# Optimization experiments

Measured on AMD Instinct MI355X. Metric: run time of the kernel, lower is better.

The kernel has to match this reference:

```python
import jax, jax.numpy as jnp
import numpy as np

WINDOW = 11
SIGMA = 1.5
K1 = 0.01
K2 = 0.03
L = 1.0


def _gauss_kernel(dtype):
    coords = jnp.arange(WINDOW, dtype=dtype) - (WINDOW - 1) / 2.0
    g = jnp.exp(-coords ** 2 / (2.0 * SIGMA ** 2))
    g = g / g.sum()
    return jnp.outer(g, g)  # [k, k]


def setup_inputs() -> dict:
    key = jax.random.key(0)
    k1, k2 = jax.random.split(key)
    B, T, H, W = 8, 16, 256, 256
    return {
        "predicted": jax.random.normal(k1, (B, T, H, W, 1), dtype=jnp.float32),
        "target": jax.random.normal(k2, (B, T, H, W, 1), dtype=jnp.float32),
    }


def reference(predicted, target):
    B, T, H, W, C = predicted.shape
    dt = predicted.dtype
    eps = jnp.asarray(1e-6, dt)

    # valid mask: samples whose target sums to zero are excluded (weighted mean)
    valid = (jnp.sum(target, axis=(1, 2, 3, 4)) != 0).astype(dt)  # [B]

    # per-sample, per-channel min-max normalization over (T, H, W)
    def norm(x):
        mn = jnp.min(x, axis=(1, 2, 3), keepdims=True)
        mx = jnp.max(x, axis=(1, 2, 3), keepdims=True)
        return (x - mn) / jnp.maximum(mx - mn, eps)

    p = norm(predicted)
    t = norm(target)

    # batch all (B,T) single-channel images through one conv: NCHW with N = B*T
    img1 = t.reshape(B * T, 1, H, W)  # original uses target as img1
    img2 = p.reshape(B * T, 1, H, W)
    kern = _gauss_kernel(dt).reshape(1, 1, WINDOW, WINDOW)
    pad = WINDOW // 2

    def conv(x):
        return jax.lax.conv_general_dilated(x, kern, (1, 1), [(pad, pad), (pad, pad)])

    mu1 = conv(img1)
    mu2 = conv(img2)
    mu1_sq = mu1 * mu1
    mu2_sq = mu2 * mu2
    mu1_mu2 = mu1 * mu2
    sigma1_sq = jnp.maximum(conv(img1 * img1) - mu1_sq, eps)
    sigma2_sq = jnp.maximum(conv(img2 * img2) - mu2_sq, eps)
    sigma12 = conv(img1 * img2) - mu1_mu2

    C1 = (K1 * L) ** 2
    C2 = (K2 * L) ** 2
    C3 = C2 / 2.0
    root = jnp.sqrt(sigma1_sq * sigma2_sq)
    luminance = (2.0 * mu1_mu2 + C1) / (mu1_sq + mu2_sq + C1)
    contrast = (2.0 * root + C2) / (sigma1_sq + sigma2_sq + C2)
    structure = (sigma12 + C3) / (root + C3)
    ssim_map = luminance * contrast * structure  # [B*T, 1, H, W]

    # per-(b,t) pixel mean, then mean over T == mean over (T,H,W)
    ssim_per_sample = ssim_map.reshape(B, T, H, W).mean(axis=(1, 2, 3))  # [B]

    n_valid = jnp.maximum(jnp.sum(valid), jnp.asarray(1.0, dt))
    loss = jnp.sum((1.0 - ssim_per_sample) * valid) / n_valid
    return loss
```

## Files before the change

### kernel.cpp

```cpp
#include <hip/hip_runtime.h>
#include <math.h>

#define BB 8
#define TT 16
#define HH 256
#define WW 256
#define NPX (TT * HH * WW)
#define CROWS 32
#define NBLK (BB * TT * (HH / CROWS))

#define P_MINP 0
#define P_MAXP 512
#define P_MINT 1024
#define P_MAXT 1536
#define P_SUMT 2048
#define WS_S   2560

typedef float v2f __attribute__((ext_vector_type(2)));

#define G0 0.0010283776f
#define G1 0.0075987582f
#define G2 0.0360008014f
#define G3 0.1093606427f
#define G4 0.2130055745f
#define G5 0.2660117857f
#define GA_(k) ((k) == 0 || (k) == 10 ? G0 : (k) == 1 || (k) == 9 ? G1 \
              : (k) == 2 || (k) == 8 ? G2 : (k) == 3 || (k) == 7 ? G3 \
              : (k) == 4 || (k) == 6 ? G4 : G5)

__global__ __launch_bounds__(256) void k_reduce(const float* __restrict__ p,
                                                const float* __restrict__ t,
                                                float* __restrict__ wsf) {
  const int b = blockIdx.x >> 6;
  const size_t base = (size_t)b * NPX + (size_t)(blockIdx.x & 63) * (NPX / 64);
  const int tid = threadIdx.x;

  float mnp = 3.4e38f, mxp = -3.4e38f, mnt = 3.4e38f, mxt = -3.4e38f, st = 0.f;
  const float4* p4 = (const float4*)(p + base);
  const float4* t4 = (const float4*)(t + base);
#pragma unroll 4
  for (int it = 0; it < 16; ++it) {
    float4 a = p4[it * 256 + tid];
    float4 c = t4[it * 256 + tid];
    mnp = fminf(mnp, fminf(fminf(a.x, a.y), fminf(a.z, a.w)));
    mxp = fmaxf(mxp, fmaxf(fmaxf(a.x, a.y), fmaxf(a.z, a.w)));
    mnt = fminf(mnt, fminf(fminf(c.x, c.y), fminf(c.z, c.w)));
    mxt = fmaxf(mxt, fmaxf(fmaxf(c.x, c.y), fmaxf(c.z, c.w)));
    st += c.x + c.y + c.z + c.w;
  }
  for (int off = 32; off > 0; off >>= 1) {
    mnp = fminf(mnp, __shfl_down(mnp, off));
    mxp = fmaxf(mxp, __shfl_down(mxp, off));
    mnt = fminf(mnt, __shfl_down(mnt, off));
    mxt = fmaxf(mxt, __shfl_down(mxt, off));
    st += __shfl_down(st, off);
  }
  __shared__ float s_mnp[4], s_mxp[4], s_mnt[4], s_mxt[4], s_st[4];
  int wave = tid >> 6, lane = tid & 63;
  if (lane == 0) {
    s_mnp[wave] = mnp; s_mxp[wave] = mxp;
    s_mnt[wave] = mnt; s_mxt[wave] = mxt; s_st[wave] = st;
  }
  __syncthreads();
  if (tid == 0) {
    for (int w = 1; w < 4; ++w) {
      mnp = fminf(mnp, s_mnp[w]); mxp = fmaxf(mxp, s_mxp[w]);
      mnt = fminf(mnt, s_mnt[w]); mxt = fmaxf(mxt, s_mxt[w]);
      st += s_st[w];
    }
    wsf[P_MINP + blockIdx.x] = mnp;
    wsf[P_MAXP + blockIdx.x] = mxp;
    wsf[P_MINT + blockIdx.x] = mnt;
    wsf[P_MAXT + blockIdx.x] = mxt;
    wsf[P_SUMT + blockIdx.x] = st;
    if (blockIdx.x == 0) wsf[WS_S] = 0.f;
  }
}

#define STEP(J) do {                                                         \
    constexpr int jj = (J);                                                  \
    constexpr int buf = jj & 1;                                              \
    constexpr int slot = jj % 11;                                            \
    const bool in = (unsigned)(ystart + jj) < (unsigned)HH;                  \
    v2f nv;                                                                  \
    nv.x = in ? fmaf(tcur, ts, tb) : 0.f;                                    \
    nv.y = in ? fmaf(pcur, ps, pb) : 0.f;                                    \
    srow[buf][x + 5] = nv;                                                   \
    if constexpr (jj < 41) {                                                 \
      const int yn = min(max(ystart + jj + 1, 0), HH - 1);                   \
      tnxt = tptr[(size_t)yn * WW + x];                                      \
      pnxt = pptr[(size_t)yn * WW + x];                                      \
    }                                                                        \
    __syncthreads();                                                         \
    v2f hmu = {0.f, 0.f}, hsq = {0.f, 0.f};                                  \
    float htp = 0.f;                                                         \
    _Pragma("unroll")                                                        \
    for (int k = 0; k < 11; ++k) {                                           \
      v2f v = srow[buf][x + k];                                              \
      v2f g2 = {GA_(k), GA_(k)};                                             \
      v2f w = g2 * v;                                                        \
      hmu = hmu + w;                                                         \
      hsq = __builtin_elementwise_fma(w, v, hsq);                            \
      htp = fmaf(w.x, v.y, htp);                                             \
    }                                                                        \
    r_mu[slot] = hmu; r_sq[slot] = hsq; r_tp[slot] = htp;                    \
    if constexpr (jj >= 10) {                                                \
      v2f vmu = {0.f, 0.f}, vsq = {0.f, 0.f};                                \
      float vtp = 0.f;                                                       \
      _Pragma("unroll")                                                      \
      for (int k = 0; k < 11; ++k) {                                         \
        const int s = (jj + 1 + k) % 11;                                     \
        v2f g2 = {GA_(k), GA_(k)};                                           \
        vmu = __builtin_elementwise_fma(g2, r_mu[s], vmu);                   \
        vsq = __builtin_elementwise_fma(g2, r_sq[s], vsq);                   \
        vtp = fmaf(GA_(k), r_tp[s], vtp);                                    \
      }                                                                      \
      float m1 = vmu.x, m2 = vmu.y;                                          \
      float mu11 = m1 * m1, mu22 = m2 * m2, m12 = m1 * m2;                   \
      float s1 = fmaxf(vsq.x - mu11, 1e-6f);                                 \
      float s2 = fmaxf(vsq.y - mu22, 1e-6f);                                 \
      float s12 = vtp - m12;                                                 \
      float root = sqrtf(s1 * s2);                                           \
      float num = fmaf(2.f, m12, C1) * fmaf(2.f, root, C2) * (s12 + C3);     \
      float den = (mu11 + mu22 + C1) * (s1 + s2 + C2) * (root + C3);         \
      acc = fmaf(num, __builtin_amdgcn_rcpf(den), acc);                      \
    }                                                                        \
    tcur = tnxt; pcur = pnxt;                                                \
    __builtin_amdgcn_sched_barrier(0);                                       \
  } while (0)

__global__ __launch_bounds__(256, 3) void k_ssim(const float* __restrict__ pred,
                                                 const float* __restrict__ targ,
                                                 float* __restrict__ wsf) {
  const int img = blockIdx.x >> 3;
  const int chunk = blockIdx.x & 7;
  const int b = img >> 4;
  const int x = threadIdx.x;
  const int y0 = chunk * CROWS;
  const float* tptr = targ + (size_t)img * (HH * WW);
  const float* pptr = pred + (size_t)img * (HH * WW);

  __shared__ float sprm[5];
  if (x < 64) {
    float mnp = wsf[P_MINP + b * 64 + x];
    float mxp = wsf[P_MAXP + b * 64 + x];
    float mnt = wsf[P_MINT + b * 64 + x];
    float mxt = wsf[P_MAXT + b * 64 + x];
    float st  = wsf[P_SUMT + b * 64 + x];
    for (int off = 32; off > 0; off >>= 1) {
      mnp = fminf(mnp, __shfl_down(mnp, off));
      mxp = fmaxf(mxp, __shfl_down(mxp, off));
      mnt = fminf(mnt, __shfl_down(mnt, off));
      mxt = fmaxf(mxt, __shfl_down(mxt, off));
      st += __shfl_down(st, off);
    }
    if (x == 0) {
      float psv = 1.f / fmaxf(mxp - mnp, 1e-6f);
      float tsv = 1.f / fmaxf(mxt - mnt, 1e-6f);
      sprm[0] = psv; sprm[1] = -mnp * psv;
      sprm[2] = tsv; sprm[3] = -mnt * tsv;
      sprm[4] = (st != 0.f) ? 1.f : 0.f;
    }
  }

  __shared__ v2f srow[2][WW + 12];
  if (x < 5) {
    v2f z = {0.f, 0.f};
    srow[0][x] = z; srow[1][x] = z;
    srow[0][WW + 5 + x] = z; srow[1][WW + 5 + x] = z;
  }
  __syncthreads();
  const float ps = sprm[0], pb = sprm[1], ts = sprm[2], tb = sprm[3];

  v2f r_mu[11], r_sq[11];
  float r_tp[11];
  float acc = 0.f;
  const int ystart = y0 - 5;
  const float C1 = 1e-4f, C2 = 9e-4f, C3 = 4.5e-4f;

  float tcur, pcur, tnxt = 0.f, pnxt = 0.f;
  {
    const int yc = min(max(ystart, 0), HH - 1);
    tcur = tptr[(size_t)yc * WW + x];
    pcur = pptr[(size_t)yc * WW + x];
  }

  STEP(0);  STEP(1);  STEP(2);  STEP(3);  STEP(4);  STEP(5);  STEP(6);
  STEP(7);  STEP(8);  STEP(9);  STEP(10); STEP(11); STEP(12); STEP(13);
  STEP(14); STEP(15); STEP(16); STEP(17); STEP(18); STEP(19); STEP(20);
  STEP(21); STEP(22); STEP(23); STEP(24); STEP(25); STEP(26); STEP(27);
  STEP(28); STEP(29); STEP(30); STEP(31); STEP(32); STEP(33); STEP(34);
  STEP(35); STEP(36); STEP(37); STEP(38); STEP(39); STEP(40); STEP(41);

  for (int off = 32; off > 0; off >>= 1) acc += __shfl_down(acc, off);
  __shared__ float sred[4];
  if ((x & 63) == 0) sred[x >> 6] = acc;
  __syncthreads();
  if (x == 0) {
    float v = sred[0] + sred[1] + sred[2] + sred[3];
    atomicAdd(&wsf[WS_S], v * sprm[4]);
  }
}

__global__ void k_loss(const float* __restrict__ wsf, float* __restrict__ out) {
  const int c = threadIdx.x;
  float sums[8];
#pragma unroll
  for (int b = 0; b < 8; ++b) sums[b] = wsf[P_SUMT + b * 64 + c];
  for (int off = 32; off > 0; off >>= 1) {
#pragma unroll
    for (int b = 0; b < 8; ++b) sums[b] += __shfl_down(sums[b], off);
  }
  if (c == 0) {
    float sv = 0.f;
#pragma unroll
    for (int b = 0; b < 8; ++b) sv += (sums[b] != 0.f) ? 1.f : 0.f;
    float S = wsf[WS_S];
    out[0] = (sv - S * (1.f / (float)NPX)) / fmaxf(sv, 1.f);
  }
}

extern "C" void kernel_launch(void* const* d_in, const int* in_sizes, int n_in,
                              void* d_out, int out_size, void* d_ws, size_t ws_size,
                              hipStream_t stream) {
  const float* pred = (const float*)d_in[0];
  const float* targ = (const float*)d_in[1];
  float* wsf = (float*)d_ws;
  float* out = (float*)d_out;

  hipLaunchKernelGGL(k_reduce, dim3(512), dim3(256), 0, stream, pred, targ, wsf);
  hipLaunchKernelGGL(k_ssim, dim3(NBLK), dim3(256), 0, stream, pred, targ, wsf);
  hipLaunchKernelGGL(k_loss, dim3(1), dim3(64), 0, stream, wsf, out);
}
```

Measured before the change: 135.7 us.

## Fuse final loss into SSIM kernel via last-block counter, raise occupancy hint

```diff
diff --git a/kernel.cpp b/kernel.cpp
--- a/kernel.cpp
+++ b/kernel.cpp
@@ -15,6 +15,7 @@
 #define P_MAXT 1536
 #define P_SUMT 2048
 #define WS_S   2560
+#define WS_CNT 2561
 
 typedef float v2f __attribute__((ext_vector_type(2)));
 
@@ -73,7 +74,10 @@
     wsf[P_MINT + blockIdx.x] = mnt;
     wsf[P_MAXT + blockIdx.x] = mxt;
     wsf[P_SUMT + blockIdx.x] = st;
-    if (blockIdx.x == 0) wsf[WS_S] = 0.f;
+    if (blockIdx.x == 0) {
+      wsf[WS_S] = 0.f;
+      ((unsigned int*)wsf)[WS_CNT] = 0u;
+    }
   }
 }
 
@@ -86,12 +90,12 @@
     nv.x = in ? fmaf(tcur, ts, tb) : 0.f;                                    \
     nv.y = in ? fmaf(pcur, ps, pb) : 0.f;                                    \
     srow[buf][x + 5] = nv;                                                   \
+    __syncthreads();                                                         \
     if constexpr (jj < 41) {                                                 \
       const int yn = min(max(ystart + jj + 1, 0), HH - 1);                   \
       tnxt = tptr[(size_t)yn * WW + x];                                      \
       pnxt = pptr[(size_t)yn * WW + x];                                      \
     }                                                                        \
-    __syncthreads();                                                         \
     v2f hmu = {0.f, 0.f}, hsq = {0.f, 0.f};                                  \
     float htp = 0.f;                                                         \
     _Pragma("unroll")                                                        \
@@ -129,9 +133,10 @@
     __builtin_amdgcn_sched_barrier(0);                                       \
   } while (0)
 
-__global__ __launch_bounds__(256, 3) void k_ssim(const float* __restrict__ pred,
+__global__ __launch_bounds__(256, 4) void k_ssim(const float* __restrict__ pred,
                                                  const float* __restrict__ targ,
-                                                 float* __restrict__ wsf) {
+                                                 float* __restrict__ wsf,
+                                                 float* __restrict__ out) {
   const int img = blockIdx.x >> 3;
   const int chunk = blockIdx.x & 7;
   const int b = img >> 4;
@@ -194,29 +199,34 @@
 
   for (int off = 32; off > 0; off >>= 1) acc += __shfl_down(acc, off);
   __shared__ float sred[4];
+  __shared__ unsigned int s_last;
   if ((x & 63) == 0) sred[x >> 6] = acc;
   __syncthreads();
   if (x == 0) {
     float v = sred[0] + sred[1] + sred[2] + sred[3];
     atomicAdd(&wsf[WS_S], v * sprm[4]);
-  }
-}
-
-__global__ void k_loss(const float* __restrict__ wsf, float* __restrict__ out) {
-  const int c = threadIdx.x;
-  float sums[8];
+    __threadfence();
+    unsigned int old = atomicAdd(((unsigned int*)wsf) + WS_CNT, 1u);
+    s_last = (old == (unsigned int)(NBLK - 1)) ? 1u : 0u;
+  }
+  __syncthreads();
+
+  if (s_last && x < 64) {
+    float sums[8];
 #pragma unroll
-  for (int b = 0; b < 8; ++b) sums[b] = wsf[P_SUMT + b * 64 + c];
-  for (int off = 32; off > 0; off >>= 1) {
+    for (int bb = 0; bb < 8; ++bb) sums[bb] = wsf[P_SUMT + bb * 64 + x];
+    for (int off = 32; off > 0; off >>= 1) {
 #pragma unroll
-    for (int b = 0; b < 8; ++b) sums[b] += __shfl_down(sums[b], off);
-  }
-  if (c == 0) {
-    float sv = 0.f;
+      for (int bb = 0; bb < 8; ++bb) sums[bb] += __shfl_down(sums[bb], off);
+    }
+    if (x == 0) {
+      __threadfence();
+      float sv = 0.f;
 #pragma unroll
-    for (int b = 0; b < 8; ++b) sv += (sums[b] != 0.f) ? 1.f : 0.f;
-    float S = wsf[WS_S];
-    out[0] = (sv - S * (1.f / (float)NPX)) / fmaxf(sv, 1.f);
+      for (int bb = 0; bb < 8; ++bb) sv += (sums[bb] != 0.f) ? 1.f : 0.f;
+      float S = atomicAdd(&wsf[WS_S], 0.f);
+      out[0] = (sv - S * (1.f / (float)NPX)) / fmaxf(sv, 1.f);
+    }
   }
 }
 
@@ -229,6 +239,5 @@
   float* out = (float*)d_out;
 
   hipLaunchKernelGGL(k_reduce, dim3(512), dim3(256), 0, stream, pred, targ, wsf);
-  hipLaunchKernelGGL(k_ssim, dim3(NBLK), dim3(256), 0, stream, pred, targ, wsf);
-  hipLaunchKernelGGL(k_loss, dim3(1), dim3(64), 0, stream, wsf, out);
+  hipLaunchKernelGGL(k_ssim, dim3(NBLK), dim3(256), 0, stream, pred, targ, wsf, out);
 }
```

Result: slower. 151.6 us (+11.7%).
